# Kernel tuning notes

Hardware: AMD Instinct MI355X
Metric: run time of the kernel (lower is better)

The kernel has to match this reference:

```python
import jax, jax.numpy as jnp
import numpy as np

B, N = 256, 131072

def setup_inputs() -> dict:
    key = jax.random.key(0)
    kx, km = jax.random.split(key)
    x = jax.random.normal(kx, (B, N), dtype=jnp.float32)
    mask = jax.random.randint(km, (B, N), 0, 2).astype(jnp.bool_)
    return {"x": x, "mask": mask}

def reference(x, mask):
    # Masked cumulative sum along dim=1: zero out masked-off entries, then scan.
    return jnp.cumsum(jnp.where(mask, x, 0.0), axis=1)
```

## Files before the change

### kernel.cpp

```cpp
#include <hip/hip_runtime.h>
#include <stdint.h>


#define B_ROWS 256
#define N_COLS 131072
#define BLOCK  256
#define VPT    8
#define TILE   (BLOCK * VPT)
#define PARTS  (N_COLS / TILE)
#define NWAVES (BLOCK / 64)
#define GRID   (B_ROWS * PARTS)

typedef float nativef4 __attribute__((ext_vector_type(4)));

__global__ __launch_bounds__(BLOCK, 8)
void masked_tile_totals(const float* __restrict__ x,
                        const int*   __restrict__ mask,
                        float*       __restrict__ totals)
{
    __shared__ float s_wsum[NWAVES];

    const int tid  = threadIdx.x;
    const int lane = tid & 63;
    const int wave = tid >> 6;
    const int bid  = blockIdx.x;
    const int row  = bid >> 6;
    const int part = bid & (PARTS - 1);

    const size_t base = (size_t)row * N_COLS + (size_t)part * TILE;
    const float4* __restrict__ x4 = (const float4*)(x + base);
    const int4*   __restrict__ m4 = (const int4*)(mask + base);

    const float4 xa = x4[tid];
    const int4   ma = m4[tid];
    const float4 xb = x4[BLOCK + tid];
    const int4   mb = m4[BLOCK + tid];

    float s = (ma.x ? xa.x : 0.0f) + (ma.y ? xa.y : 0.0f)
            + (ma.z ? xa.z : 0.0f) + (ma.w ? xa.w : 0.0f)
            + (mb.x ? xb.x : 0.0f) + (mb.y ? xb.y : 0.0f)
            + (mb.z ? xb.z : 0.0f) + (mb.w ? xb.w : 0.0f);

    #pragma unroll
    for (int o = 32; o > 0; o >>= 1)
        s += __shfl_xor(s, o, 64);

    if (lane == 0) s_wsum[wave] = s;
    __syncthreads();
    if (tid == 0)
        totals[bid] = s_wsum[0] + s_wsum[1] + s_wsum[2] + s_wsum[3];
}

__device__ __forceinline__ float wave_incl_scan(float v, int lane) {
    #pragma unroll
    for (int d = 1; d < 64; d <<= 1) {
        const float y = __shfl_up(v, d, 64);
        if (lane >= d) v += y;
    }
    return v;
}

__global__ __launch_bounds__(BLOCK, 8)
void masked_cumsum_scan(const float* __restrict__ x,
                        const int*   __restrict__ mask,
                        const float* __restrict__ totals,
                        float*       __restrict__ out)
{
    __shared__ float s_wsum[2][NWAVES];
    __shared__ float s_prefix;

    const int tid  = threadIdx.x;
    const int lane = tid & 63;
    const int wave = tid >> 6;
    const int bid  = blockIdx.x;
    const int row  = bid >> 6;
    const int part = bid & (PARTS - 1);

    const size_t base = (size_t)row * N_COLS + (size_t)part * TILE;
    const float4* __restrict__ x4 = (const float4*)(x + base);
    const int4*   __restrict__ m4 = (const int4*)(mask + base);
    nativef4*     __restrict__ o4 = (nativef4*)(out + base);

    const float4 xa = x4[tid];
    const int4   ma = m4[tid];
    const float4 xb = x4[BLOCK + tid];
    const int4   mb = m4[BLOCK + tid];
    const float  tl = (wave == 0) ? totals[(row << 6) + lane] : 0.0f;

    const float a0 = ma.x ? xa.x : 0.0f;
    const float a1 = ma.y ? xa.y : 0.0f;
    const float a2 = ma.z ? xa.z : 0.0f;
    const float a3 = ma.w ? xa.w : 0.0f;
    const float sa0 = a0;
    const float sa1 = sa0 + a1;
    const float sa2 = sa1 + a2;
    const float sa3 = sa2 + a3;
    const float inclA  = wave_incl_scan(sa3, lane);
    const float wexclA = inclA - sa3;
    if (lane == 63) s_wsum[0][wave] = inclA;

    const float b0 = mb.x ? xb.x : 0.0f;
    const float b1 = mb.y ? xb.y : 0.0f;
    const float b2 = mb.z ? xb.z : 0.0f;
    const float b3 = mb.w ? xb.w : 0.0f;
    const float sb0 = b0;
    const float sb1 = sb0 + b1;
    const float sb2 = sb1 + b2;
    const float sb3 = sb2 + b3;
    const float inclB  = wave_incl_scan(sb3, lane);
    const float wexclB = inclB - sb3;
    if (lane == 63) s_wsum[1][wave] = inclB;

    if (wave == 0) {
        float c = (lane < part) ? tl : 0.0f;
        #pragma unroll
        for (int o = 32; o > 0; o >>= 1)
            c += __shfl_xor(c, o, 64);
        if (lane == 0) s_prefix = c;
    }
    __syncthreads();

    float offA = 0.0f, totA = 0.0f, offB = 0.0f;
    #pragma unroll
    for (int w = 0; w < NWAVES; ++w) {
        const float va = s_wsum[0][w];
        const float vb = s_wsum[1][w];
        if (w < wave) { offA += va; offB += vb; }
        totA += va;
    }
    const float pre   = s_prefix;
    const float baseA = pre + offA + wexclA;
    const float baseB = pre + totA + offB + wexclB;

    nativef4 ra, rb;
    ra.x = baseA + sa0;
    ra.y = baseA + sa1;
    ra.z = baseA + sa2;
    ra.w = baseA + sa3;
    rb.x = baseB + sb0;
    rb.y = baseB + sb1;
    rb.z = baseB + sb2;
    rb.w = baseB + sb3;
    __builtin_nontemporal_store(ra, &o4[tid]);
    __builtin_nontemporal_store(rb, &o4[BLOCK + tid]);
}

#define FB_BLOCK  1024
#define FB_VEC    4
#define FB_TILE   (FB_BLOCK * FB_VEC)
#define FB_NTILES (N_COLS / FB_TILE)
#define FB_NWAVES (FB_BLOCK / 64)

__global__ __launch_bounds__(FB_BLOCK)
void masked_cumsum_fallback(const float* __restrict__ x,
                            const int* __restrict__ mask,
                            float* __restrict__ out) {
    __shared__ float waveSums[2][FB_NWAVES];

    const int row  = blockIdx.x;
    const int tid  = threadIdx.x;
    const int lane = tid & 63;
    const int wave = tid >> 6;

    const size_t rowBase = (size_t)row * N_COLS;
    const float4* __restrict__ x4 = (const float4*)(x + rowBase);
    const int4*   __restrict__ m4 = (const int4*)(mask + rowBase);
    float4*       __restrict__ o4 = (float4*)(out + rowBase);

    float carry = 0.0f;
    float4 xv = x4[tid];
    int4   mv = m4[tid];

    for (int t = 0; t < FB_NTILES; ++t) {
        const float4 cx = xv;
        const int4   cm = mv;
        if (t + 1 < FB_NTILES) {
            const int nidx = (t + 1) * FB_BLOCK + tid;
            xv = x4[nidx];
            mv = m4[nidx];
        }
        const float v0 = cm.x ? cx.x : 0.0f;
        const float v1 = cm.y ? cx.y : 0.0f;
        const float v2 = cm.z ? cx.z : 0.0f;
        const float v3 = cm.w ? cx.w : 0.0f;
        const float s0 = v0;
        const float s1 = s0 + v1;
        const float s2 = s1 + v2;
        const float s3 = s2 + v3;
        const float tsum = s3;

        float incl = tsum;
        #pragma unroll
        for (int d = 1; d < 64; d <<= 1) {
            const float y = __shfl_up(incl, d, 64);
            if (lane >= d) incl += y;
        }
        const float waveExcl = incl - tsum;

        if (lane == 63) waveSums[t & 1][wave] = incl;
        __syncthreads();

        float waveOff = 0.0f, tileTot = 0.0f;
        #pragma unroll
        for (int w = 0; w < FB_NWAVES; ++w) {
            const float s = waveSums[t & 1][w];
            if (w < wave) waveOff += s;
            tileTot += s;
        }

        const float base = carry + waveOff + waveExcl;
        float4 r;
        r.x = base + s0;
        r.y = base + s1;
        r.z = base + s2;
        r.w = base + s3;
        o4[t * FB_BLOCK + tid] = r;

        carry += tileTot;
    }
}

extern "C" void kernel_launch(void* const* d_in, const int* in_sizes, int n_in,
                              void* d_out, int out_size, void* d_ws, size_t ws_size,
                              hipStream_t stream) {
    const float* x    = (const float*)d_in[0];
    const int*   mask = (const int*)d_in[1];
    float*       out  = (float*)d_out;
    (void)in_sizes; (void)n_in; (void)out_size;

    const size_t need = (size_t)GRID * sizeof(float);
    if (d_ws != nullptr && ws_size >= need) {
        float* totals = (float*)d_ws;
        masked_tile_totals<<<GRID, BLOCK, 0, stream>>>(x, mask, totals);
        masked_cumsum_scan<<<GRID, BLOCK, 0, stream>>>(x, mask, totals, out);
    } else {
        masked_cumsum_fallback<<<B_ROWS, FB_BLOCK, 0, stream>>>(x, mask, out);
    }
}
```

Before: 347.7 us.

## Process eight chunks per block with a register-prefetched serial loop in both passes

Each block of the reduce-then-scan now covers a segment of eight 2048-element chunks instead of one chunk. The grid shrinks from 16384 to 2048 blocks and each block loops with next-iteration loads prefetched into registers. In the scan pass a block carries a running prefix across its chunks, and the cross-segment prefix is summed serially from eight totals. This cuts per-block launch and prefix overhead but leaves fewer blocks to hide memory latency, and the scan loop adds a barrier per iteration.

```diff
diff --git a/kernel.cpp b/kernel.cpp
--- a/kernel.cpp
+++ b/kernel.cpp
@@ -2,54 +2,18 @@
 #include <stdint.h>
 
 
-#define B_ROWS 256
-#define N_COLS 131072
-#define BLOCK  256
-#define VPT    8
-#define TILE   (BLOCK * VPT)
-#define PARTS  (N_COLS / TILE)
-#define NWAVES (BLOCK / 64)
-#define GRID   (B_ROWS * PARTS)
+#define B_ROWS  256
+#define N_COLS  131072
+#define BLOCK   256
+#define VPT     8
+#define CHUNK   (BLOCK * VPT)
+#define ITERS   8
+#define SEG     (CHUNK * ITERS)
+#define SEGS    (N_COLS / SEG)
+#define NWAVES  (BLOCK / 64)
+#define GRID_AB (B_ROWS * SEGS)
 
 typedef float nativef4 __attribute__((ext_vector_type(4)));
-
-__global__ __launch_bounds__(BLOCK, 8)
-void masked_tile_totals(const float* __restrict__ x,
-                        const int*   __restrict__ mask,
-                        float*       __restrict__ totals)
-{
-    __shared__ float s_wsum[NWAVES];
-
-    const int tid  = threadIdx.x;
-    const int lane = tid & 63;
-    const int wave = tid >> 6;
-    const int bid  = blockIdx.x;
-    const int row  = bid >> 6;
-    const int part = bid & (PARTS - 1);
-
-    const size_t base = (size_t)row * N_COLS + (size_t)part * TILE;
-    const float4* __restrict__ x4 = (const float4*)(x + base);
-    const int4*   __restrict__ m4 = (const int4*)(mask + base);
-
-    const float4 xa = x4[tid];
-    const int4   ma = m4[tid];
-    const float4 xb = x4[BLOCK + tid];
-    const int4   mb = m4[BLOCK + tid];
-
-    float s = (ma.x ? xa.x : 0.0f) + (ma.y ? xa.y : 0.0f)
-            + (ma.z ? xa.z : 0.0f) + (ma.w ? xa.w : 0.0f)
-            + (mb.x ? xb.x : 0.0f) + (mb.y ? xb.y : 0.0f)
-            + (mb.z ? xb.z : 0.0f) + (mb.w ? xb.w : 0.0f);
-
-    #pragma unroll
-    for (int o = 32; o > 0; o >>= 1)
-        s += __shfl_xor(s, o, 64);
-
-    if (lane == 0) s_wsum[wave] = s;
-    __syncthreads();
-    if (tid == 0)
-        totals[bid] = s_wsum[0] + s_wsum[1] + s_wsum[2] + s_wsum[3];
-}
 
 __device__ __forceinline__ float wave_incl_scan(float v, int lane) {
     #pragma unroll
@@ -61,88 +25,148 @@
 }
 
 __global__ __launch_bounds__(BLOCK, 8)
-void masked_cumsum_scan(const float* __restrict__ x,
-                        const int*   __restrict__ mask,
-                        const float* __restrict__ totals,
-                        float*       __restrict__ out)
+void seg_totals(const float* __restrict__ x,
+                const int*   __restrict__ mask,
+                float*       __restrict__ totals)
 {
-    __shared__ float s_wsum[2][NWAVES];
-    __shared__ float s_prefix;
+    __shared__ float s_wsum[NWAVES];
 
     const int tid  = threadIdx.x;
     const int lane = tid & 63;
     const int wave = tid >> 6;
     const int bid  = blockIdx.x;
-    const int row  = bid >> 6;
-    const int part = bid & (PARTS - 1);
-
-    const size_t base = (size_t)row * N_COLS + (size_t)part * TILE;
+    const int row  = bid >> 3;
+    const int seg  = bid & (SEGS - 1);
+
+    const size_t base = (size_t)row * N_COLS + (size_t)seg * SEG;
+    const float4* __restrict__ x4 = (const float4*)(x + base);
+    const int4*   __restrict__ m4 = (const int4*)(mask + base);
+
+    float acc = 0.0f;
+
+    float4 xa = x4[tid];
+    int4   ma = m4[tid];
+    float4 xb = x4[BLOCK + tid];
+    int4   mb = m4[BLOCK + tid];
+
+    for (int t = 0; t < ITERS; ++t) {
+        const float4 cxa = xa; const int4 cma = ma;
+        const float4 cxb = xb; const int4 cmb = mb;
+        if (t + 1 < ITERS) {
+            const int nb = (t + 1) * (2 * BLOCK) + tid;
+            xa = x4[nb];         ma = m4[nb];
+            xb = x4[nb + BLOCK]; mb = m4[nb + BLOCK];
+        }
+        acc += (cma.x ? cxa.x : 0.0f) + (cma.y ? cxa.y : 0.0f)
+             + (cma.z ? cxa.z : 0.0f) + (cma.w ? cxa.w : 0.0f)
+             + (cmb.x ? cxb.x : 0.0f) + (cmb.y ? cxb.y : 0.0f)
+             + (cmb.z ? cxb.z : 0.0f) + (cmb.w ? cxb.w : 0.0f);
+    }
+
+    #pragma unroll
+    for (int o = 32; o > 0; o >>= 1)
+        acc += __shfl_xor(acc, o, 64);
+
+    if (lane == 0) s_wsum[wave] = acc;
+    __syncthreads();
+    if (tid == 0)
+        totals[bid] = s_wsum[0] + s_wsum[1] + s_wsum[2] + s_wsum[3];
+}
+
+__global__ __launch_bounds__(BLOCK, 8)
+void seg_scan(const float* __restrict__ x,
+              const int*   __restrict__ mask,
+              const float* __restrict__ totals,
+              float*       __restrict__ out)
+{
+    __shared__ float s_ws[2][2][NWAVES];
+
+    const int tid  = threadIdx.x;
+    const int lane = tid & 63;
+    const int wave = tid >> 6;
+    const int bid  = blockIdx.x;
+    const int row  = bid >> 3;
+    const int seg  = bid & (SEGS - 1);
+
+    const size_t base = (size_t)row * N_COLS + (size_t)seg * SEG;
     const float4* __restrict__ x4 = (const float4*)(x + base);
     const int4*   __restrict__ m4 = (const int4*)(mask + base);
     nativef4*     __restrict__ o4 = (nativef4*)(out + base);
 
-    const float4 xa = x4[tid];
-    const int4   ma = m4[tid];
-    const float4 xb = x4[BLOCK + tid];
-    const int4   mb = m4[BLOCK + tid];
-    const float  tl = (wave == 0) ? totals[(row << 6) + lane] : 0.0f;
-
-    const float a0 = ma.x ? xa.x : 0.0f;
-    const float a1 = ma.y ? xa.y : 0.0f;
-    const float a2 = ma.z ? xa.z : 0.0f;
-    const float a3 = ma.w ? xa.w : 0.0f;
-    const float sa0 = a0;
-    const float sa1 = sa0 + a1;
-    const float sa2 = sa1 + a2;
-    const float sa3 = sa2 + a3;
-    const float inclA  = wave_incl_scan(sa3, lane);
-    const float wexclA = inclA - sa3;
-    if (lane == 63) s_wsum[0][wave] = inclA;
-
-    const float b0 = mb.x ? xb.x : 0.0f;
-    const float b1 = mb.y ? xb.y : 0.0f;
-    const float b2 = mb.z ? xb.z : 0.0f;
-    const float b3 = mb.w ? xb.w : 0.0f;
-    const float sb0 = b0;
-    const float sb1 = sb0 + b1;
-    const float sb2 = sb1 + b2;
-    const float sb3 = sb2 + b3;
-    const float inclB  = wave_incl_scan(sb3, lane);
-    const float wexclB = inclB - sb3;
-    if (lane == 63) s_wsum[1][wave] = inclB;
-
-    if (wave == 0) {
-        float c = (lane < part) ? tl : 0.0f;
+    float carry = 0.0f;
+    const float* __restrict__ trow = totals + (row << 3);
+    for (int i = 0; i < seg; ++i) carry += trow[i];
+
+    float4 xa = x4[tid];
+    int4   ma = m4[tid];
+    float4 xb = x4[BLOCK + tid];
+    int4   mb = m4[BLOCK + tid];
+
+    for (int t = 0; t < ITERS; ++t) {
+        const float4 cxa = xa; const int4 cma = ma;
+        const float4 cxb = xb; const int4 cmb = mb;
+        if (t + 1 < ITERS) {
+            const int nb = (t + 1) * (2 * BLOCK) + tid;
+            xa = x4[nb];         ma = m4[nb];
+            xb = x4[nb + BLOCK]; mb = m4[nb + BLOCK];
+        }
+
+        const float a0 = cma.x ? cxa.x : 0.0f;
+        const float a1 = cma.y ? cxa.y : 0.0f;
+        const float a2 = cma.z ? cxa.z : 0.0f;
+        const float a3 = cma.w ? cxa.w : 0.0f;
+        const float sa0 = a0;
+        const float sa1 = sa0 + a1;
+        const float sa2 = sa1 + a2;
+        const float sa3 = sa2 + a3;
+        const float inclA  = wave_incl_scan(sa3, lane);
+        const float wexclA = inclA - sa3;
+
+        const float b0 = cmb.x ? cxb.x : 0.0f;
+        const float b1 = cmb.y ? cxb.y : 0.0f;
+        const float b2 = cmb.z ? cxb.z : 0.0f;
+        const float b3 = cmb.w ? cxb.w : 0.0f;
+        const float sb0 = b0;
+        const float sb1 = sb0 + b1;
+        const float sb2 = sb1 + b2;
+        const float sb3 = sb2 + b3;
+        const float inclB  = wave_incl_scan(sb3, lane);
+        const float wexclB = inclB - sb3;
+
+        if (lane == 63) {
+            s_ws[t & 1][0][wave] = inclA;
+            s_ws[t & 1][1][wave] = inclB;
+        }
+        __syncthreads();
+
+        float offA = 0.0f, totA = 0.0f, offB = 0.0f, totB = 0.0f;
         #pragma unroll
-        for (int o = 32; o > 0; o >>= 1)
-            c += __shfl_xor(c, o, 64);
-        if (lane == 0) s_prefix = c;
-    }
-    __syncthreads();
-
-    float offA = 0.0f, totA = 0.0f, offB = 0.0f;
-    #pragma unroll
-    for (int w = 0; w < NWAVES; ++w) {
-        const float va = s_wsum[0][w];
-        const float vb = s_wsum[1][w];
-        if (w < wave) { offA += va; offB += vb; }
-        totA += va;
-    }
-    const float pre   = s_prefix;
-    const float baseA = pre + offA + wexclA;
-    const float baseB = pre + totA + offB + wexclB;
-
-    nativef4 ra, rb;
-    ra.x = baseA + sa0;
-    ra.y = baseA + sa1;
-    ra.z = baseA + sa2;
-    ra.w = baseA + sa3;
-    rb.x = baseB + sb0;
-    rb.y = baseB + sb1;
-    rb.z = baseB + sb2;
-    rb.w = baseB + sb3;
-    __builtin_nontemporal_store(ra, &o4[tid]);
-    __builtin_nontemporal_store(rb, &o4[BLOCK + tid]);
+        for (int w = 0; w < NWAVES; ++w) {
+            const float va = s_ws[t & 1][0][w];
+            const float vb = s_ws[t & 1][1][w];
+            if (w < wave) { offA += va; offB += vb; }
+            totA += va;
+            totB += vb;
+        }
+
+        const float baseA = carry + offA + wexclA;
+        const float baseB = carry + totA + offB + wexclB;
+
+        nativef4 ra, rb;
+        ra.x = baseA + sa0;
+        ra.y = baseA + sa1;
+        ra.z = baseA + sa2;
+        ra.w = baseA + sa3;
+        rb.x = baseB + sb0;
+        rb.y = baseB + sb1;
+        rb.z = baseB + sb2;
+        rb.w = baseB + sb3;
+        const int ob = t * (2 * BLOCK) + tid;
+        __builtin_nontemporal_store(ra, &o4[ob]);
+        __builtin_nontemporal_store(rb, &o4[ob + BLOCK]);
+
+        carry += totA + totB;
+    }
 }
 
 #define FB_BLOCK  1024
@@ -228,11 +252,11 @@
     float*       out  = (float*)d_out;
     (void)in_sizes; (void)n_in; (void)out_size;
 
-    const size_t need = (size_t)GRID * sizeof(float);
+    const size_t need = (size_t)GRID_AB * sizeof(float);
     if (d_ws != nullptr && ws_size >= need) {
         float* totals = (float*)d_ws;
-        masked_tile_totals<<<GRID, BLOCK, 0, stream>>>(x, mask, totals);
-        masked_cumsum_scan<<<GRID, BLOCK, 0, stream>>>(x, mask, totals, out);
+        seg_totals<<<GRID_AB, BLOCK, 0, stream>>>(x, mask, totals);
+        seg_scan<<<GRID_AB, BLOCK, 0, stream>>>(x, mask, totals, out);
     } else {
         masked_cumsum_fallback<<<B_ROWS, FB_BLOCK, 0, stream>>>(x, mask, out);
     }
```

New measurement: 356.7 us. +2.6%, slower.
